# Kernel optimization log

Measured on AMD Instinct MI355X. Metric: run time of the kernel, lower is better.

Reference implementation:

```python
import jax, jax.numpy as jnp
import numpy as np
from jax import lax

EPS = 1e-5
B, CIN, H, W = 2, 2048, 32, 32

def conv2d(x, w, pad):
    return lax.conv_general_dilated(x, w, (1, 1), [(pad, pad), (pad, pad)],
                                    dimension_numbers=('NCHW', 'OIHW', 'NCHW'))

def batchnorm(x, gamma, beta):
    mu = jnp.mean(x, axis=(0, 2, 3), keepdims=True)
    var = jnp.var(x, axis=(0, 2, 3), keepdims=True)
    return (x - mu) * lax.rsqrt(var + EPS) * gamma.reshape(1, -1, 1, 1) + beta.reshape(1, -1, 1, 1)

def deform_conv(x, w_off, w_m, w, k, dil, pad):
    # modulated deformable conv v2: offset conv (3x3) -> 2*k*k, modulation conv -> k*k
    b, c, h, wd = x.shape
    n = k * k
    off = conv2d(x, w_off, 1)                        # [B,2N,H,W]
    mod = jax.nn.sigmoid(conv2d(x, w_m, 1))          # [B,N,H,W]
    off_y = jnp.transpose(off[:, :n], (0, 2, 3, 1))  # [B,H,W,N]
    off_x = jnp.transpose(off[:, n:], (0, 2, 3, 1))
    mod = jnp.transpose(mod, (0, 2, 3, 1))           # [B,H,W,N]
    x_pad = jnp.pad(x, ((0, 0), (0, 0), (pad, pad), (pad, pad)))
    hp, wp = h + 2 * pad, wd + 2 * pad
    taps = (jnp.arange(k) * dil).astype(x.dtype)
    gy = jnp.arange(h, dtype=x.dtype)[:, None] + taps[None, :]   # [H,k] base y in padded coords
    gx = jnp.arange(wd, dtype=x.dtype)[:, None] + taps[None, :]  # [W,k]
    py = (gy[None, :, None, :, None] + off_y.reshape(b, h, wd, k, k)).reshape(b, h, wd, n)
    px = (gx[None, None, :, None, :] + off_x.reshape(b, h, wd, k, k)).reshape(b, h, wd, n)
    py = jnp.clip(py, 0.0, hp - 1)
    px = jnp.clip(px, 0.0, wp - 1)
    y0 = jnp.floor(py); x0 = jnp.floor(px)
    wy = py - y0; wx = px - x0
    y0i = jnp.clip(y0.astype(jnp.int32), 0, hp - 1)
    x0i = jnp.clip(x0.astype(jnp.int32), 0, wp - 1)
    y1i = jnp.clip(y0i + 1, 0, hp - 1)
    x1i = jnp.clip(x0i + 1, 0, wp - 1)
    xf = x_pad.reshape(b, c, hp * wp)
    def gather(yi, xi):
        idx = (yi * wp + xi).reshape(b, -1)               # [B, H*W*N]
        return jax.vmap(lambda f, i: f[:, i])(xf, idx)    # [B, C, H*W*N]
    wy = wy.reshape(b, 1, -1); wx = wx.reshape(b, 1, -1)
    val = ((1 - wy) * (1 - wx) * gather(y0i, x0i)
         + (1 - wy) * wx       * gather(y0i, x1i)
         + wy       * (1 - wx) * gather(y1i, x0i)
         + wy       * wx       * gather(y1i, x1i))
    val = (val * mod.reshape(b, 1, -1)).reshape(b, c, h, wd, n)
    return jnp.einsum('bchwn,ocn->bohw', val, w.reshape(w.shape[0], c, n))

def dspp_forward(x, woff1, wm1, w1, g1, b1, woff2, wm2, w2, g2, b2,
                 woff3, wm3, w3, g3, b3, woff4, wm4, w4, g4, b4,
                 wpool, gp, bp, wfuse, gf, bf):
    x1 = jax.nn.relu(batchnorm(deform_conv(x, woff1, wm1, w1, 1, 1, 0), g1, b1))
    x2 = jax.nn.relu(batchnorm(deform_conv(x, woff2, wm2, w2, 3, 6, 6), g2, b2))
    x3 = jax.nn.relu(batchnorm(deform_conv(x, woff3, wm3, w3, 3, 12, 12), g3, b3))
    x4 = jax.nn.relu(batchnorm(deform_conv(x, woff4, wm4, w4, 3, 18, 18), g4, b4))
    gap = jnp.mean(x, axis=(2, 3))                    # [B,Cin] global avg pool
    p = jnp.einsum('bc,oc->bo', gap, wpool)           # 1x1 conv
    mu = jnp.mean(p, axis=0); var = jnp.var(p, axis=0)
    p = jax.nn.relu((p - mu) * lax.rsqrt(var + EPS) * gp + bp)
    x5 = jnp.broadcast_to(p[:, :, None, None], x4.shape)  # bilinear upsample from 1x1 == broadcast
    cat = jnp.concatenate([x1, x2, x3, x4, x5], axis=1)   # [B,1280,H,W]
    out = jnp.einsum('bchw,oc->bohw', cat, wfuse)
    out = jax.nn.relu(batchnorm(out, gf, bf))
    return out  # dropout is identity at inference


def setup_inputs() -> dict:
    key = jax.random.key(0)
    ks = jax.random.split(key, 16)
    dt = jnp.float32
    def kaiming(k, shape):
        fan_in = int(np.prod(shape[1:]))
        return jax.random.normal(k, shape, dt) * np.float32(np.sqrt(2.0 / fan_in))
    inp = {'x': jax.random.normal(ks[0], (B, CIN, H, W), dt)}
    specs = [(1, 'woff1', 'wm1', 'w1', 'g1', 'b1'),
             (3, 'woff2', 'wm2', 'w2', 'g2', 'b2'),
             (3, 'woff3', 'wm3', 'w3', 'g3', 'b3'),
             (3, 'woff4', 'wm4', 'w4', 'g4', 'b4')]
    i = 1
    for k, no, nm, nw, ng, nb in specs:
        n = k * k
        inp[no] = jax.random.normal(ks[i], (2 * n, CIN, 3, 3), dt) * 0.01; i += 1
        inp[nm] = jax.random.normal(ks[i], (n, CIN, 3, 3), dt) * 0.01; i += 1
        inp[nw] = kaiming(ks[i], (256, CIN, k, k)); i += 1
        inp[ng] = jnp.ones((256,), dt)
        inp[nb] = jnp.zeros((256,), dt)
    inp['wpool'] = kaiming(ks[i], (256, CIN)); i += 1
    inp['gp'] = jnp.ones((256,), dt); inp['bp'] = jnp.zeros((256,), dt)
    inp['wfuse'] = kaiming(ks[i], (256, 1280))
    inp['gf'] = jnp.ones((256,), dt); inp['bf'] = jnp.zeros((256,), dt)
    return inp


def reference(x, woff1, wm1, w1, g1, b1, woff2, wm2, w2, g2, b2,
              woff3, wm3, w3, g3, b3, woff4, wm4, w4, g4, b4,
              wpool, gp, bp, wfuse, gf, bf):
    return dspp_forward(x, woff1, wm1, w1, g1, b1, woff2, wm2, w2, g2, b2,
                        woff3, wm3, w3, g3, b3, woff4, wm4, w4, g4, b4,
                        wpool, gp, bp, wfuse, gf, bf)
```

## Files before the change

### kernel.cpp

```cpp
#include <hip/hip_runtime.h>
#include <hip/hip_fp16.h>
#include <cstdint>
#include <cstddef>

#define EPSV 1e-5f

typedef _Float16 f16x8 __attribute__((ext_vector_type(8)));
typedef float f32x4 __attribute__((ext_vector_type(4)));

__device__ __forceinline__ short f2h(float f) {
    _Float16 h = (_Float16)f;
    union { _Float16 h; short s; } u; u.h = h; return u.s;
}
__device__ __forceinline__ __half2 u2h2(unsigned u) {
    union { unsigned u; __half2 h; } x; x.u = u; return x.h;
}
__device__ __forceinline__ unsigned packh2(float w) {
    _Float16 h = (_Float16)w;
    union { _Float16 h; unsigned short s; } u; u.h = h;
    return (unsigned)u.s * 0x10001u;
}

__global__ void k_zero(float4* p, int n4) {
    int i = blockIdx.x * blockDim.x + threadIdx.x;
    int stride = gridDim.x * blockDim.x;
    for (; i < n4; i += stride) p[i] = float4{0.f, 0.f, 0.f, 0.f};
}

__global__ void k_xpose(const float* __restrict__ x, short* __restrict__ xT) {
    int hw0 = blockIdx.x * 64, c0 = blockIdx.y * 64, b = blockIdx.z;
    __shared__ short tile[64][72];
    int t = threadIdx.x;
    const float* xb = x + (size_t)b * 2048 * 1024;
    int hwi = t & 63, cr = t >> 6;
    #pragma unroll
    for (int r = 0; r < 16; r++) {
        int cl = cr + r * 4;
        tile[hwi][cl] = f2h(xb[(size_t)(c0 + cl) * 1024 + hw0 + hwi]);
    }
    __syncthreads();
    short* xTb = xT + (size_t)b * 1024 * 2048;
    int ci = t & 63, hr = t >> 6;
    #pragma unroll
    for (int r = 0; r < 16; r++) {
        int hwr = hr + r * 4;
        xTb[(size_t)(hw0 + hwr) * 2048 + c0 + ci] = tile[hwr][ci];
    }
}

__global__ void k_convw1(const float* __restrict__ w1, short* __restrict__ A1) {
    int i = blockIdx.x * 256 + threadIdx.x;
    if (i < 256 * 2048) A1[i] = f2h(w1[i]);
}

__global__ void k_convw9(const float* w2, const float* w3, const float* w4,
                         short* A2, short* A3, short* A4) {
    int o = blockIdx.x, cch = blockIdx.y, br = blockIdx.z;
    const float* src = br == 0 ? w2 : br == 1 ? w3 : w4;
    short* dst = br == 0 ? A2 : br == 1 ? A3 : A4;
    __shared__ short lds[4608];
    int t = threadIdx.x;
    const float* basep = src + ((size_t)o * 2048 + cch * 512) * 9;
    #pragma unroll
    for (int s = 0; s < 18; s++) {
        int idx = s * 256 + t;
        int c = idx / 9, jj = idx - c * 9;
        lds[jj * 512 + c] = f2h(basep[idx]);
    }
    __syncthreads();
    short* dbase = dst + (size_t)o * 18432 + cch * 512;
    #pragma unroll
    for (int s = 0; s < 18; s++) {
        int idx = s * 256 + t;
        int jj = idx >> 9, c = idx & 511;
        dbase[(size_t)jj * 2048 + c] = lds[idx];
    }
}

__global__ void k_convoff(const float* woff1, const float* wm1, const float* woff2, const float* wm2,
                          const float* woff3, const float* wm3, const float* woff4, const float* wm4,
                          short* Aoff) {
    int ch = blockIdx.x, cch = blockIdx.y;
    int t = threadIdx.x;
    short* dbase = Aoff + (size_t)ch * 18432 + cch * 512;
    if (ch >= 84) {
        #pragma unroll
        for (int s = 0; s < 18; s++) {
            int idx = s * 256 + t;
            int jj = idx >> 9, c = idx & 511;
            dbase[(size_t)jj * 2048 + c] = 0;
        }
        return;
    }
    const float* src; int oc;
    if (ch < 2)       { src = woff1; oc = ch; }
    else if (ch == 2) { src = wm1;   oc = 0; }
    else if (ch < 21) { src = woff2; oc = ch - 3; }
    else if (ch < 30) { src = wm2;   oc = ch - 21; }
    else if (ch < 48) { src = woff3; oc = ch - 30; }
    else if (ch < 57) { src = wm3;   oc = ch - 48; }
    else if (ch < 75) { src = woff4; oc = ch - 57; }
    else              { src = wm4;   oc = ch - 75; }
    __shared__ short lds[4608];
    const float* basep = src + ((size_t)oc * 2048 + cch * 512) * 9;
    #pragma unroll
    for (int s = 0; s < 18; s++) {
        int idx = s * 256 + t;
        int c = idx / 9, jj = idx - c * 9;
        lds[jj * 512 + c] = f2h(basep[idx]);
    }
    __syncthreads();
    #pragma unroll
    for (int s = 0; s < 18; s++) {
        int idx = s * 256 + t;
        int jj = idx >> 9, c = idx & 511;
        dbase[(size_t)jj * 2048 + c] = lds[idx];
    }
}

__global__ void k_afuse(const float* wfuse, short* Af) {
    int i = blockIdx.x * 256 + threadIdx.x;
    if (i < 256 * 1280) Af[i] = f2h(wfuse[i]);
}

__global__ void k_shtab(int* dtab0) {
    int i = blockIdx.x * 256 + threadIdx.x;
    if (i >= 9 * 2048) return;
    int j = i >> 11, p = i & 2047;
    int hw = p & 1023, h = hw >> 5, w = hw & 31;
    int y = h + j / 3 - 1, xx = w + j % 3 - 1;
    bool v = (y >= 0 && y < 32 && xx >= 0 && xx < 32);
    int4 ii = {v ? y * 32 + xx : 0, 0, 0, 0};
    uint4 ww = {v ? packh2(1.f) : 0u, 0u, 0u, 0u};
    ((int4*)dtab0)[(size_t)i * 2] = ii;
    ((uint4*)dtab0)[(size_t)i * 2 + 1] = ww;
}

__global__ void k_sample(const float* OM, int* dtabi) {
    int i = blockIdx.x * 256 + threadIdx.x;
    if (i >= 57344) return;
    int br, j, p;
    if (i < 2048) { br = 0; j = 0; p = i; }
    else { int r = i - 2048; br = 1 + r / 18432; r %= 18432; j = r >> 11; p = r & 2047; }
    const int dil_[4] = {1, 6, 12, 18};
    const int pad_[4] = {0, 6, 12, 18};
    const int cho_[4] = {0, 3, 30, 57};
    const int chm_[4] = {2, 21, 48, 75};
    const int tbo_[4] = {0, 2048, 20480, 38912};
    int J = br ? 9 : 1;
    int dil = dil_[br], pad = pad_[br];
    int hw = p & 1023, h = hw >> 5, w = hw & 31;
    float offy = OM[(size_t)(cho_[br] + j) * 2048 + p];
    float offx = OM[(size_t)(cho_[br] + J + j) * 2048 + p];
    float mz   = OM[(size_t)(chm_[br] + j) * 2048 + p];
    float m = 1.f / (1.f + expf(-mz));
    int ky = j / 3, kx = j - ky * 3;
    float fh = (float)(h + ky * dil) + offy;
    float fw = (float)(w + kx * dil) + offx;
    int limi = 31 + 2 * pad;
    float lim = (float)limi;
    fh = fminf(fmaxf(fh, 0.f), lim);
    fw = fminf(fmaxf(fw, 0.f), lim);
    float y0f = floorf(fh), x0f = floorf(fw);
    float wy = fh - y0f, wx = fw - x0f;
    int y0 = (int)y0f, x0 = (int)x0f;
    int y1 = min(y0 + 1, limi), x1 = min(x0 + 1, limi);
    int4 ii; uint4 ww;
    {
        int yo = y0 - pad, xo = x0 - pad;
        bool v = ((unsigned)yo < 32u) && ((unsigned)xo < 32u);
        ii.x = v ? yo * 32 + xo : 0; ww.x = v ? packh2((1.f - wy) * (1.f - wx) * m) : 0u;
    }
    {
        int yo = y0 - pad, xo = x1 - pad;
        bool v = ((unsigned)yo < 32u) && ((unsigned)xo < 32u);
        ii.y = v ? yo * 32 + xo : 0; ww.y = v ? packh2((1.f - wy) * wx * m) : 0u;
    }
    {
        int yo = y1 - pad, xo = x0 - pad;
        bool v = ((unsigned)yo < 32u) && ((unsigned)xo < 32u);
        ii.z = v ? yo * 32 + xo : 0; ww.z = v ? packh2(wy * (1.f - wx) * m) : 0u;
    }
    {
        int yo = y1 - pad, xo = x1 - pad;
        bool v = ((unsigned)yo < 32u) && ((unsigned)xo < 32u);
        ii.w = v ? yo * 32 + xo : 0; ww.w = v ? packh2(wy * wx * m) : 0u;
    }
    int ent = tbo_[br] + j * 2048 + p;
    ((int4*)dtabi)[(size_t)ent * 2] = ii;
    ((uint4*)dtabi)[(size_t)ent * 2 + 1] = ww;
}

template <int WM>
__device__ __forceinline__ void gemm_gather_f16(
    const short* __restrict__ A, const int* __restrict__ tab,
    const short* __restrict__ xT, float* __restrict__ C,
    int K, int kbeg, int kend, int nbase)
{
    constexpr int TPB = WM * 128;
    constexpr int TPP = TPB / 128;
    constexpr int CPT = 32 / TPP;
    constexpr int NG = CPT / 8;
    __shared__ __align__(16) short At[WM * 64][40];
    __shared__ __align__(16) short Bt[128][40];
    int t = threadIdx.x;
    f32x4 acc[4][4] = {};

    int p = t / TPP;
    int q = (t % TPP) * CPT;
    int pg = nbase + p;
    int bb = nbase >> 10;
    int jj = kbeg >> 11;
    const int4* te = (const int4*)tab + ((size_t)jj * 2048 + pg) * 2;
    int4 ii = te[0];
    uint4 wp = *(const uint4*)(te + 1);
    __half2 wt0 = u2h2(wp.x), wt1 = u2h2(wp.y), wt2 = u2h2(wp.z), wt3 = u2h2(wp.w);
    const short* xbase = xT + (size_t)bb * 1024 * 2048 + q;
    const short* rp0 = xbase + (size_t)ii.x * 2048;
    const short* rp1 = xbase + (size_t)ii.y * 2048;
    const short* rp2 = xbase + (size_t)ii.z * 2048;
    const short* rp3 = xbase + (size_t)ii.w * 2048;

    int arow = t >> 1;
    int aseg = (t & 1) * 16;
    const short* Ar = A + (size_t)arow * K + aseg;

    int lane = t & 63, wv = t >> 6;
    int mq = (wv >> 1) * 64, nq = (wv & 1) * 64;
    int lm = lane & 15, quad = lane >> 4;

    for (int k0 = kbeg; k0 < kend; k0 += 32) {
        *(uint4*)&At[arow][aseg]     = *(const uint4*)(Ar + k0);
        *(uint4*)&At[arow][aseg + 8] = *(const uint4*)(Ar + k0 + 8);
        {
            int ck = k0 & 2047;
            #pragma unroll
            for (int g = 0; g < NG; g++) {
                __half2 a0 = u2h2(0u), a1 = u2h2(0u), a2 = u2h2(0u), a3 = u2h2(0u);
                int cko = ck + g * 8;
                uint4 d0 = *(const uint4*)(rp0 + cko);
                a0 = __hfma2(u2h2(d0.x), wt0, a0); a1 = __hfma2(u2h2(d0.y), wt0, a1);
                a2 = __hfma2(u2h2(d0.z), wt0, a2); a3 = __hfma2(u2h2(d0.w), wt0, a3);
                uint4 d1 = *(const uint4*)(rp1 + cko);
                a0 = __hfma2(u2h2(d1.x), wt1, a0); a1 = __hfma2(u2h2(d1.y), wt1, a1);
                a2 = __hfma2(u2h2(d1.z), wt1, a2); a3 = __hfma2(u2h2(d1.w), wt1, a3);
                uint4 d2 = *(const uint4*)(rp2 + cko);
                a0 = __hfma2(u2h2(d2.x), wt2, a0); a1 = __hfma2(u2h2(d2.y), wt2, a1);
                a2 = __hfma2(u2h2(d2.z), wt2, a2); a3 = __hfma2(u2h2(d2.w), wt2, a3);
                uint4 d3 = *(const uint4*)(rp3 + cko);
                a0 = __hfma2(u2h2(d3.x), wt3, a0); a1 = __hfma2(u2h2(d3.y), wt3, a1);
                a2 = __hfma2(u2h2(d3.z), wt3, a2); a3 = __hfma2(u2h2(d3.w), wt3, a3);
                union { __half2 h[4]; uint4 u; } pk;
                pk.h[0] = a0; pk.h[1] = a1; pk.h[2] = a2; pk.h[3] = a3;
                *(uint4*)&Bt[p][q + g * 8] = pk.u;
            }
        }
        __syncthreads();
        f16x8 af[4], bfv[4];
        #pragma unroll
        for (int f = 0; f < 4; f++) {
            af[f]  = *(const f16x8*)&At[mq + f * 16 + lm][quad * 8];
            bfv[f] = *(const f16x8*)&Bt[nq + f * 16 + lm][quad * 8];
        }
        #pragma unroll
        for (int fm = 0; fm < 4; fm++)
            #pragma unroll
            for (int fn = 0; fn < 4; fn++)
                acc[fm][fn] = __builtin_amdgcn_mfma_f32_16x16x32_f16(af[fm], bfv[fn], acc[fm][fn], 0, 0, 0);
        __syncthreads();
    }
    #pragma unroll
    for (int fm = 0; fm < 4; fm++) {
        int row0 = mq + fm * 16 + quad * 4;
        #pragma unroll
        for (int fn = 0; fn < 4; fn++) {
            int col = nbase + nq + fn * 16 + lm;
            #pragma unroll
            for (int r = 0; r < 4; r++)
                atomicAdd(&C[(size_t)(row0 + r) * 2048 + col], acc[fm][fn][r]);
        }
    }
}

__global__ __launch_bounds__(256) void k_ogemm(const short* __restrict__ Aoff,
                                               const int* __restrict__ dtab0,
                                               const short* __restrict__ xT,
                                               float* __restrict__ offmod) {
    int kbeg = blockIdx.z * 1024;
    gemm_gather_f16<2>(Aoff, dtab0, xT, offmod, 18432, kbeg, kbeg + 1024, blockIdx.x * 128);
}

__global__ __launch_bounds__(512) void k_dgemm(const short* __restrict__ Aall,
                                               const int* __restrict__ dtab,
                                               const short* __restrict__ xT,
                                               float* __restrict__ ypre) {
    int z = blockIdx.z;
    int br, kbeg;
    if (z < 2) { br = 0; kbeg = z * 1024; }
    else { int zz = z - 2; br = 1 + zz / 18; kbeg = (zz % 18) * 1024; }
    const size_t aoffs[4] = {0, 524288, 524288 + 4718592, 524288 + 2 * (size_t)4718592};
    const int tbo[4] = {0, 2048, 20480, 38912};
    int K = br ? 18432 : 2048;
    gemm_gather_f16<4>(Aall + aoffs[br], dtab + (size_t)tbo[br] * 8, xT,
                       ypre + (size_t)br * 524288, K, kbeg, kbeg + 1024, blockIdx.x * 128);
}

__global__ __launch_bounds__(256) void k_fgemm(const short* __restrict__ A,
                                               const short* __restrict__ Bp,
                                               float* __restrict__ C) {
    __shared__ __align__(16) short At[128][40];
    __shared__ __align__(16) short Bt[128][40];
    int t = threadIdx.x;
    int nbase = blockIdx.x * 128, mbase = blockIdx.y * 128;
    int kbeg = blockIdx.z * 160, kend = kbeg + 160;
    const int K = 1280;
    f32x4 acc[4][4] = {};
    int lane = t & 63, wv = t >> 6;
    int mq = (wv >> 1) * 64, nq = (wv & 1) * 64;
    int lm = lane & 15, quad = lane >> 4;
    for (int k0 = kbeg; k0 < kend; k0 += 32) {
        int row = t >> 2, seg = t & 3;
        *(uint4*)&At[row][seg * 8] = *(const uint4*)(A + (size_t)(mbase + row) * K + k0 + seg * 8);
        *(uint4*)&At[row + 64][seg * 8] = *(const uint4*)(A + (size_t)(mbase + row + 64) * K + k0 + seg * 8);
        *(uint4*)&Bt[row][seg * 8] = *(const uint4*)(Bp + (size_t)(nbase + row) * K + k0 + seg * 8);
        *(uint4*)&Bt[row + 64][seg * 8] = *(const uint4*)(Bp + (size_t)(nbase + row + 64) * K + k0 + seg * 8);
        __syncthreads();
        f16x8 af[4], bfv[4];
        #pragma unroll
        for (int f = 0; f < 4; f++) {
            af[f]  = *(const f16x8*)&At[mq + f * 16 + lm][quad * 8];
            bfv[f] = *(const f16x8*)&Bt[nq + f * 16 + lm][quad * 8];
        }
        #pragma unroll
        for (int fm = 0; fm < 4; fm++)
            #pragma unroll
            for (int fn = 0; fn < 4; fn++)
                acc[fm][fn] = __builtin_amdgcn_mfma_f32_16x16x32_f16(af[fm], bfv[fn], acc[fm][fn], 0, 0, 0);
        __syncthreads();
    }
    #pragma unroll
    for (int fm = 0; fm < 4; fm++) {
        int row0 = mbase + mq + fm * 16 + quad * 4;
        #pragma unroll
        for (int fn = 0; fn < 4; fn++) {
            int col = nbase + nq + fn * 16 + lm;
            #pragma unroll
            for (int r = 0; r < 4; r++)
                atomicAdd(&C[(size_t)(row0 + r) * 2048 + col], acc[fm][fn][r]);
        }
    }
}

__global__ void k_bnstats(const float* Y0, const float* Y1, const float* Y2, const float* Y3,
                          const float* g0, const float* g1, const float* g2, const float* g3,
                          const float* b0, const float* b1, const float* b2, const float* b3,
                          float* S) {
    int br = blockIdx.y;
    const float* Y = br == 0 ? Y0 : br == 1 ? Y1 : br == 2 ? Y2 : Y3;
    const float* g = br == 0 ? g0 : br == 1 ? g1 : br == 2 ? g2 : g3;
    const float* b = br == 0 ? b0 : br == 1 ? b1 : br == 2 ? b2 : b3;
    float* so = S + (size_t)br * 512;
    int o = blockIdx.x, t = threadIdx.x;
    const float* row = Y + (size_t)o * 2048;
    float s = 0.f, ss = 0.f;
    for (int i = t; i < 2048; i += 256) { float v = row[i]; s += v; ss += v * v; }
    #pragma unroll
    for (int off = 32; off; off >>= 1) { s += __shfl_down(s, off); ss += __shfl_down(ss, off); }
    __shared__ float ls[4], lss[4];
    int wv = t >> 6;
    if ((t & 63) == 0) { ls[wv] = s; lss[wv] = ss; }
    __syncthreads();
    if (t == 0) {
        s = ls[0] + ls[1] + ls[2] + ls[3];
        ss = lss[0] + lss[1] + lss[2] + lss[3];
        float mu = s * (1.f / 2048.f);
        float var = ss * (1.f / 2048.f) - mu * mu;
        float sc = g[o] * rsqrtf(var + EPSV);
        so[o] = sc;
        so[256 + o] = b[o] - mu * sc;
    }
}

__global__ void k_gap(const float* X, float* gap) {
    int bc = blockIdx.x;
    const float* row = X + (size_t)bc * 1024;
    int t = threadIdx.x;
    float s = row[t] + row[t + 256] + row[t + 512] + row[t + 768];
    #pragma unroll
    for (int off = 32; off; off >>= 1) s += __shfl_down(s, off);
    __shared__ float ls[4];
    if ((t & 63) == 0) ls[t >> 6] = s;
    __syncthreads();
    if (t == 0) gap[bc] = (ls[0] + ls[1] + ls[2] + ls[3]) * (1.f / 1024.f);
}

__global__ void k_pool(const float* gap, const float* wpool, const float* gp, const float* bp,
                       float* pfin) {
    int o = blockIdx.x, t = threadIdx.x;
    float s0 = 0.f, s1 = 0.f;
    const float* wr = wpool + (size_t)o * 2048;
    for (int c = t; c < 2048; c += 256) {
        float wv = wr[c];
        s0 += wv * gap[c];
        s1 += wv * gap[2048 + c];
    }
    #pragma unroll
    for (int off = 32; off; off >>= 1) { s0 += __shfl_down(s0, off); s1 += __shfl_down(s1, off); }
    __shared__ float l0[4], l1[4];
    int wv_ = t >> 6;
    if ((t & 63) == 0) { l0[wv_] = s0; l1[wv_] = s1; }
    __syncthreads();
    if (t == 0) {
        float p0 = l0[0] + l0[1] + l0[2] + l0[3];
        float p1 = l1[0] + l1[1] + l1[2] + l1[3];
        float mu = 0.5f * (p0 + p1);
        float d0 = p0 - mu, d1 = p1 - mu;
        float var = 0.5f * (d0 * d0 + d1 * d1);
        float r = rsqrtf(var + EPSV);
        pfin[o]       = fmaxf(d0 * r * gp[o] + bp[o], 0.f);
        pfin[256 + o] = fmaxf(d1 * r * gp[o] + bp[o], 0.f);
    }
}

__global__ void k_xcat(const float* __restrict__ ypre, const float* __restrict__ S,
                       const float* __restrict__ pfin, short* __restrict__ xcat) {
    int p0 = blockIdx.x * 64, ct = blockIdx.y;
    int t = threadIdx.x;
    if (ct >= 16) {
        int c0 = 1024 + (ct - 16) * 64;
        int ci = t & 63, pr = t >> 6;
        #pragma unroll
        for (int r = 0; r < 16; r++) {
            int pw = p0 + pr + r * 4;
            int b = pw >> 10;
            xcat[(size_t)pw * 1280 + c0 + ci] = f2h(pfin[b * 256 + (c0 - 1024) + ci]);
        }
        return;
    }
    __shared__ short tile[64][72];
    int c0 = ct * 64;
    int pi = t & 63, cr = t >> 6;
    #pragma unroll
    for (int r = 0; r < 16; r++) {
        int cl = cr + r * 4;
        int cg = c0 + cl;
        int br = cg >> 8, cc = cg & 255;
        float sc = S[br * 512 + cc], sh = S[br * 512 + 256 + cc];
        float v = fmaxf(ypre[(size_t)cg * 2048 + p0 + pi] * sc + sh, 0.f);
        tile[pi][cl] = f2h(v);
    }
    __syncthreads();
    int ci = t & 63, pr = t >> 6;
    #pragma unroll
    for (int r = 0; r < 16; r++) {
        int pw = pr + r * 4;
        xcat[(size_t)(p0 + pw) * 1280 + c0 + ci] = tile[pw][ci];
    }
}

__global__ void k_final(const float* outpre, const float* S, float* dout) {
    int i = blockIdx.x * 256 + threadIdx.x;
    int hw = i & 1023, o = (i >> 10) & 255, b = i >> 18;
    float v = outpre[(size_t)o * 2048 + b * 1024 + hw] * S[o] + S[256 + o];
    dout[i] = fmaxf(v, 0.f);
}

extern "C" void kernel_launch(void* const* d_in, const int* in_sizes, int n_in,
                              void* d_out, int out_size, void* d_ws, size_t ws_size,
                              hipStream_t stream) {
    const float* x     = (const float*)d_in[0];
    const float* woff1 = (const float*)d_in[1];
    const float* wm1   = (const float*)d_in[2];
    const float* w1    = (const float*)d_in[3];
    const float* g1    = (const float*)d_in[4];
    const float* b1    = (const float*)d_in[5];
    const float* woff2 = (const float*)d_in[6];
    const float* wm2   = (const float*)d_in[7];
    const float* w2    = (const float*)d_in[8];
    const float* g2    = (const float*)d_in[9];
    const float* b2    = (const float*)d_in[10];
    const float* woff3 = (const float*)d_in[11];
    const float* wm3   = (const float*)d_in[12];
    const float* w3    = (const float*)d_in[13];
    const float* g3    = (const float*)d_in[14];
    const float* b3    = (const float*)d_in[15];
    const float* woff4 = (const float*)d_in[16];
    const float* wm4   = (const float*)d_in[17];
    const float* w4    = (const float*)d_in[18];
    const float* g4    = (const float*)d_in[19];
    const float* b4    = (const float*)d_in[20];
    const float* wpool = (const float*)d_in[21];
    const float* gp    = (const float*)d_in[22];
    const float* bp    = (const float*)d_in[23];
    const float* wfuse = (const float*)d_in[24];
    const float* gf    = (const float*)d_in[25];
    const float* bf    = (const float*)d_in[26];

    char* ws = (char*)d_ws;
    size_t off = 0;
    auto alloc = [&](size_t bytes) {
        off = (off + 255) & ~(size_t)255;
        size_t o = off; off += bytes; return o;
    };
    size_t off_offmod = alloc(128 * 2048 * 4);
    size_t off_ypre   = alloc((size_t)4 * 256 * 2048 * 4);
    size_t off_outpre = alloc(256 * 2048 * 4);
    size_t off_A1     = alloc((size_t)256 * 2048 * 2);
    size_t off_A2     = alloc((size_t)256 * 18432 * 2);
    size_t off_A3     = alloc((size_t)256 * 18432 * 2);
    size_t off_A4     = alloc((size_t)256 * 18432 * 2);
    size_t off_Aoff   = alloc((size_t)128 * 18432 * 2);
    size_t off_Afuse  = alloc((size_t)256 * 1280 * 2);
    size_t off_xcat   = alloc((size_t)2048 * 1280 * 2);
    size_t off_xT     = alloc((size_t)2 * 1024 * 2048 * 2);
    size_t off_dtab0  = alloc((size_t)9 * 2048 * 32);
    size_t off_dtab   = alloc((size_t)57344 * 32);
    size_t off_scsh   = alloc((size_t)4 * 512 * 4);
    size_t off_scshf  = alloc((size_t)512 * 4);
    size_t off_gap    = alloc((size_t)4096 * 4);
    size_t off_pfin   = alloc((size_t)512 * 4);
    (void)ws_size; (void)in_sizes; (void)n_in; (void)out_size;

    float* offmod = (float*)(ws + off_offmod);
    float* ypre   = (float*)(ws + off_ypre);
    float* outpre = (float*)(ws + off_outpre);
    short* Aall   = (short*)(ws + off_A1);
    short* A1     = (short*)(ws + off_A1);
    short* A2     = (short*)(ws + off_A2);
    short* A3     = (short*)(ws + off_A3);
    short* A4     = (short*)(ws + off_A4);
    short* Aoff   = (short*)(ws + off_Aoff);
    short* Afuse  = (short*)(ws + off_Afuse);
    short* xcat   = (short*)(ws + off_xcat);
    short* xT     = (short*)(ws + off_xT);
    int*   dtab0  = (int*)(ws + off_dtab0);
    int*   dtab   = (int*)(ws + off_dtab);
    float* scsh   = (float*)(ws + off_scsh);
    float* scshf  = (float*)(ws + off_scshf);
    float* gapb   = (float*)(ws + off_gap);
    float* pfin   = (float*)(ws + off_pfin);

    k_zero<<<2048, 256, 0, stream>>>((float4*)(ws + off_offmod), 720896);
    k_xpose<<<dim3(16, 32, 2), 256, 0, stream>>>(x, xT);
    k_convw1<<<2048, 256, 0, stream>>>(w1, A1);
    k_convw9<<<dim3(256, 4, 3), 256, 0, stream>>>(w2, w3, w4, A2, A3, A4);
    k_convoff<<<dim3(128, 4), 256, 0, stream>>>(woff1, wm1, woff2, wm2, woff3, wm3, woff4, wm4, Aoff);
    k_afuse<<<1280, 256, 0, stream>>>(wfuse, Afuse);
    k_shtab<<<72, 256, 0, stream>>>(dtab0);
    k_ogemm<<<dim3(16, 1, 18), 256, 0, stream>>>(Aoff, dtab0, xT, offmod);
    k_sample<<<224, 256, 0, stream>>>(offmod, dtab);
    k_dgemm<<<dim3(16, 1, 56), 512, 0, stream>>>(Aall, dtab, xT, ypre);
    k_bnstats<<<dim3(256, 4), 256, 0, stream>>>(ypre, ypre + 524288, ypre + 2 * 524288, ypre + 3 * 524288,
                                                g1, g2, g3, g4, b1, b2, b3, b4, scsh);
    k_gap<<<4096, 256, 0, stream>>>(x, gapb);
    k_pool<<<256, 256, 0, stream>>>(gapb, wpool, gp, bp, pfin);
    k_xcat<<<dim3(32, 20), 256, 0, stream>>>(ypre, scsh, pfin, xcat);
    k_fgemm<<<dim3(16, 2, 8), 256, 0, stream>>>(Afuse, xcat, outpre);
    k_bnstats<<<dim3(256, 1), 256, 0, stream>>>(outpre, outpre, outpre, outpre,
                                                gf, gf, gf, gf, bf, bf, bf, bf, scshf);
    k_final<<<2048, 256, 0, stream>>>(outpre, scshf, (float*)d_out);
}
```

Baseline: 428.0 us.

## Fuse prep kernels, register-prefetch gather GEMM, specialize offset GEMM taps

Merges the zeroing, weight conversion, transpose, shift-table and global-average-pool kernels into one launch, and folds the pooling branch into the batchnorm stats kernel, cutting the number of launches. The gather GEMM now double-buffers A and gathered-x loads in registers so the next stage's global loads overlap the MFMAs. It also adds a single-tap specialization for the offset GEMM, whose table only has one valid tap, so it skips three gathers. The offset GEMM's K split is doubled and occupancy hints are added, at the cost of higher register pressure and more atomic partial sums.

```diff
diff --git a/kernel.cpp b/kernel.cpp
--- a/kernel.cpp
+++ b/kernel.cpp
@@ -7,6 +7,7 @@
 
 typedef _Float16 f16x8 __attribute__((ext_vector_type(8)));
 typedef float f32x4 __attribute__((ext_vector_type(4)));
+typedef short short4v __attribute__((ext_vector_type(4)));
 
 __device__ __forceinline__ short f2h(float f) {
     _Float16 h = (_Float16)f;
@@ -21,119 +22,143 @@
     return (unsigned)u.s * 0x10001u;
 }
 
-__global__ void k_zero(float4* p, int n4) {
-    int i = blockIdx.x * blockDim.x + threadIdx.x;
-    int stride = gridDim.x * blockDim.x;
-    for (; i < n4; i += stride) p[i] = float4{0.f, 0.f, 0.f, 0.f};
-}
-
-__global__ void k_xpose(const float* __restrict__ x, short* __restrict__ xT) {
-    int hw0 = blockIdx.x * 64, c0 = blockIdx.y * 64, b = blockIdx.z;
-    __shared__ short tile[64][72];
-    int t = threadIdx.x;
-    const float* xb = x + (size_t)b * 2048 * 1024;
-    int hwi = t & 63, cr = t >> 6;
-    #pragma unroll
-    for (int r = 0; r < 16; r++) {
-        int cl = cr + r * 4;
-        tile[hwi][cl] = f2h(xb[(size_t)(c0 + cl) * 1024 + hw0 + hwi]);
-    }
-    __syncthreads();
-    short* xTb = xT + (size_t)b * 1024 * 2048;
-    int ci = t & 63, hr = t >> 6;
-    #pragma unroll
-    for (int r = 0; r < 16; r++) {
-        int hwr = hr + r * 4;
-        xTb[(size_t)(hw0 + hwr) * 2048 + c0 + ci] = tile[hwr][ci];
-    }
-}
-
-__global__ void k_convw1(const float* __restrict__ w1, short* __restrict__ A1) {
-    int i = blockIdx.x * 256 + threadIdx.x;
-    if (i < 256 * 2048) A1[i] = f2h(w1[i]);
-}
-
-__global__ void k_convw9(const float* w2, const float* w3, const float* w4,
-                         short* A2, short* A3, short* A4) {
-    int o = blockIdx.x, cch = blockIdx.y, br = blockIdx.z;
-    const float* src = br == 0 ? w2 : br == 1 ? w3 : w4;
-    short* dst = br == 0 ? A2 : br == 1 ? A3 : A4;
-    __shared__ short lds[4608];
-    int t = threadIdx.x;
-    const float* basep = src + ((size_t)o * 2048 + cch * 512) * 9;
-    #pragma unroll
-    for (int s = 0; s < 18; s++) {
-        int idx = s * 256 + t;
-        int c = idx / 9, jj = idx - c * 9;
-        lds[jj * 512 + c] = f2h(basep[idx]);
-    }
-    __syncthreads();
-    short* dbase = dst + (size_t)o * 18432 + cch * 512;
-    #pragma unroll
-    for (int s = 0; s < 18; s++) {
-        int idx = s * 256 + t;
-        int jj = idx >> 9, c = idx & 511;
-        dbase[(size_t)jj * 2048 + c] = lds[idx];
-    }
-}
-
-__global__ void k_convoff(const float* woff1, const float* wm1, const float* woff2, const float* wm2,
-                          const float* woff3, const float* wm3, const float* woff4, const float* wm4,
-                          short* Aoff) {
-    int ch = blockIdx.x, cch = blockIdx.y;
-    int t = threadIdx.x;
-    short* dbase = Aoff + (size_t)ch * 18432 + cch * 512;
-    if (ch >= 84) {
+__global__ __launch_bounds__(256) void k_prep(
+    const float* __restrict__ x, short* __restrict__ xT,
+    const float* __restrict__ w1, short* __restrict__ A1,
+    const float* __restrict__ wfuse, short* __restrict__ Af,
+    int* __restrict__ dtab0,
+    const float* __restrict__ woff1, const float* __restrict__ wm1,
+    const float* __restrict__ woff2, const float* __restrict__ wm2,
+    const float* __restrict__ woff3, const float* __restrict__ wm3,
+    const float* __restrict__ woff4, const float* __restrict__ wm4,
+    short* __restrict__ Aoff,
+    const float* __restrict__ w2, const float* __restrict__ w3, const float* __restrict__ w4,
+    short* __restrict__ A2, short* __restrict__ A3, short* __restrict__ A4,
+    float4* __restrict__ zbase, float* __restrict__ gap)
+{
+    __shared__ short lds9[4608];
+    __shared__ float lsg[4];
+    int bx = blockIdx.x, t = threadIdx.x;
+    if (bx < 1024) {
+        for (int i = bx * 256 + t; i < 720896; i += 262144)
+            zbase[i] = float4{0.f, 0.f, 0.f, 0.f};
+        return;
+    }
+    if (bx < 1536) {
+        int i4 = (bx - 1024) * 256 + t;
+        float4 v = ((const float4*)w1)[i4];
+        ((short4v*)A1)[i4] = short4v{f2h(v.x), f2h(v.y), f2h(v.z), f2h(v.w)};
+        return;
+    }
+    if (bx < 1856) {
+        int i4 = (bx - 1536) * 256 + t;
+        float4 v = ((const float4*)wfuse)[i4];
+        ((short4v*)Af)[i4] = short4v{f2h(v.x), f2h(v.y), f2h(v.z), f2h(v.w)};
+        return;
+    }
+    if (bx < 1928) {
+        int i = (bx - 1856) * 256 + t;
+        if (i >= 9 * 2048) return;
+        int j = i >> 11, p = i & 2047;
+        int hw = p & 1023, h = hw >> 5, w = hw & 31;
+        int y = h + j / 3 - 1, xx = w + j % 3 - 1;
+        bool v = (y >= 0 && y < 32 && xx >= 0 && xx < 32);
+        int4 ii = {v ? y * 32 + xx : 0, 0, 0, 0};
+        uint4 ww = {v ? packh2(1.f) : 0u, 0u, 0u, 0u};
+        ((int4*)dtab0)[(size_t)i * 2] = ii;
+        ((uint4*)dtab0)[(size_t)i * 2 + 1] = ww;
+        return;
+    }
+    if (bx < 2440) {
+        int qb = bx - 1928;
+        int ch = qb >> 2, cch = qb & 3;
+        short* dbase = Aoff + (size_t)ch * 18432 + cch * 512;
+        if (ch >= 84) {
+            #pragma unroll
+            for (int s = 0; s < 18; s++) {
+                int idx = s * 256 + t;
+                int jj = idx >> 9, c = idx & 511;
+                dbase[(size_t)jj * 2048 + c] = 0;
+            }
+            return;
+        }
+        const float* src; int oc;
+        if (ch < 2)       { src = woff1; oc = ch; }
+        else if (ch == 2) { src = wm1;   oc = 0; }
+        else if (ch < 21) { src = woff2; oc = ch - 3; }
+        else if (ch < 30) { src = wm2;   oc = ch - 21; }
+        else if (ch < 48) { src = woff3; oc = ch - 30; }
+        else if (ch < 57) { src = wm3;   oc = ch - 48; }
+        else if (ch < 75) { src = woff4; oc = ch - 57; }
+        else              { src = wm4;   oc = ch - 75; }
+        const float* basep = src + ((size_t)oc * 2048 + cch * 512) * 9;
+        #pragma unroll
+        for (int s = 0; s < 18; s++) {
+            int idx = s * 256 + t;
+            int c = idx / 9, jj = idx - c * 9;
+            lds9[jj * 512 + c] = f2h(basep[idx]);
+        }
+        __syncthreads();
         #pragma unroll
         for (int s = 0; s < 18; s++) {
             int idx = s * 256 + t;
             int jj = idx >> 9, c = idx & 511;
-            dbase[(size_t)jj * 2048 + c] = 0;
-        }
-        return;
-    }
-    const float* src; int oc;
-    if (ch < 2)       { src = woff1; oc = ch; }
-    else if (ch == 2) { src = wm1;   oc = 0; }
-    else if (ch < 21) { src = woff2; oc = ch - 3; }
-    else if (ch < 30) { src = wm2;   oc = ch - 21; }
-    else if (ch < 48) { src = woff3; oc = ch - 30; }
-    else if (ch < 57) { src = wm3;   oc = ch - 48; }
-    else if (ch < 75) { src = woff4; oc = ch - 57; }
-    else              { src = wm4;   oc = ch - 75; }
-    __shared__ short lds[4608];
-    const float* basep = src + ((size_t)oc * 2048 + cch * 512) * 9;
-    #pragma unroll
-    for (int s = 0; s < 18; s++) {
-        int idx = s * 256 + t;
-        int c = idx / 9, jj = idx - c * 9;
-        lds[jj * 512 + c] = f2h(basep[idx]);
-    }
-    __syncthreads();
-    #pragma unroll
-    for (int s = 0; s < 18; s++) {
-        int idx = s * 256 + t;
-        int jj = idx >> 9, c = idx & 511;
-        dbase[(size_t)jj * 2048 + c] = lds[idx];
-    }
-}
-
-__global__ void k_afuse(const float* wfuse, short* Af) {
-    int i = blockIdx.x * 256 + threadIdx.x;
-    if (i < 256 * 1280) Af[i] = f2h(wfuse[i]);
-}
-
-__global__ void k_shtab(int* dtab0) {
-    int i = blockIdx.x * 256 + threadIdx.x;
-    if (i >= 9 * 2048) return;
-    int j = i >> 11, p = i & 2047;
-    int hw = p & 1023, h = hw >> 5, w = hw & 31;
-    int y = h + j / 3 - 1, xx = w + j % 3 - 1;
-    bool v = (y >= 0 && y < 32 && xx >= 0 && xx < 32);
-    int4 ii = {v ? y * 32 + xx : 0, 0, 0, 0};
-    uint4 ww = {v ? packh2(1.f) : 0u, 0u, 0u, 0u};
-    ((int4*)dtab0)[(size_t)i * 2] = ii;
-    ((uint4*)dtab0)[(size_t)i * 2 + 1] = ww;
+            dbase[(size_t)jj * 2048 + c] = lds9[idx];
+        }
+        return;
+    }
+    if (bx < 5512) {
+        int qb = bx - 2440;
+        int o = qb & 255, cch = (qb >> 8) & 3, br = qb >> 10;
+        const float* src = br == 0 ? w2 : br == 1 ? w3 : w4;
+        short* dst = br == 0 ? A2 : br == 1 ? A3 : A4;
+        const float* basep = src + ((size_t)o * 2048 + cch * 512) * 9;
+        #pragma unroll
+        for (int s = 0; s < 18; s++) {
+            int idx = s * 256 + t;
+            int c = idx / 9, jj = idx - c * 9;
+            lds9[jj * 512 + c] = f2h(basep[idx]);
+        }
+        __syncthreads();
+        short* dbase = dst + (size_t)o * 18432 + cch * 512;
+        #pragma unroll
+        for (int s = 0; s < 18; s++) {
+            int idx = s * 256 + t;
+            int jj = idx >> 9, c = idx & 511;
+            dbase[(size_t)jj * 2048 + c] = lds9[idx];
+        }
+        return;
+    }
+    if (bx < 6536) {
+        int qb = bx - 5512;
+        int hw0 = (qb & 15) * 64, c0 = ((qb >> 4) & 31) * 64, b = qb >> 9;
+        const float* xb = x + (size_t)b * 2048 * 1024;
+        int hwi = t & 63, cr = t >> 6;
+        #pragma unroll
+        for (int r = 0; r < 16; r++) {
+            int cl = cr + r * 4;
+            lds9[hwi * 72 + cl] = f2h(xb[(size_t)(c0 + cl) * 1024 + hw0 + hwi]);
+        }
+        __syncthreads();
+        short* xTb = xT + (size_t)b * 1024 * 2048;
+        int ci = t & 63, hr = t >> 6;
+        #pragma unroll
+        for (int r = 0; r < 16; r++) {
+            int hwr = hr + r * 4;
+            xTb[(size_t)(hw0 + hwr) * 2048 + c0 + ci] = lds9[hwr * 72 + ci];
+        }
+        return;
+    }
+    {
+        int bc = bx - 6536;
+        const float* row = x + (size_t)bc * 1024;
+        float s = row[t] + row[t + 256] + row[t + 512] + row[t + 768];
+        #pragma unroll
+        for (int off = 32; off; off >>= 1) s += __shfl_down(s, off);
+        if ((t & 63) == 0) lsg[t >> 6] = s;
+        __syncthreads();
+        if (t == 0) gap[bc] = (lsg[0] + lsg[1] + lsg[2] + lsg[3]) * (1.f / 1024.f);
+    }
 }
 
 __global__ void k_sample(const float* OM, int* dtabi) {
@@ -191,14 +216,13 @@
     ((uint4*)dtabi)[(size_t)ent * 2 + 1] = ww;
 }
 
-template <int WM>
+template <int WM, int NTAP>
 __device__ __forceinline__ void gemm_gather_f16(
     const short* __restrict__ A, const int* __restrict__ tab,
     const short* __restrict__ xT, float* __restrict__ C,
     int K, int kbeg, int kend, int nbase)
 {
-    constexpr int TPB = WM * 128;
-    constexpr int TPP = TPB / 128;
+    constexpr int TPP = WM;
     constexpr int CPT = 32 / TPP;
     constexpr int NG = CPT / 8;
     __shared__ __align__(16) short At[WM * 64][40];
@@ -229,46 +253,81 @@
     int mq = (wv >> 1) * 64, nq = (wv & 1) * 64;
     int lm = lane & 15, quad = lane >> 4;
 
-    for (int k0 = kbeg; k0 < kend; k0 += 32) {
-        *(uint4*)&At[arow][aseg]     = *(const uint4*)(Ar + k0);
-        *(uint4*)&At[arow][aseg + 8] = *(const uint4*)(Ar + k0 + 8);
-        {
-            int ck = k0 & 2047;
-            #pragma unroll
-            for (int g = 0; g < NG; g++) {
-                __half2 a0 = u2h2(0u), a1 = u2h2(0u), a2 = u2h2(0u), a3 = u2h2(0u);
-                int cko = ck + g * 8;
-                uint4 d0 = *(const uint4*)(rp0 + cko);
-                a0 = __hfma2(u2h2(d0.x), wt0, a0); a1 = __hfma2(u2h2(d0.y), wt0, a1);
-                a2 = __hfma2(u2h2(d0.z), wt0, a2); a3 = __hfma2(u2h2(d0.w), wt0, a3);
-                uint4 d1 = *(const uint4*)(rp1 + cko);
-                a0 = __hfma2(u2h2(d1.x), wt1, a0); a1 = __hfma2(u2h2(d1.y), wt1, a1);
-                a2 = __hfma2(u2h2(d1.z), wt1, a2); a3 = __hfma2(u2h2(d1.w), wt1, a3);
-                uint4 d2 = *(const uint4*)(rp2 + cko);
-                a0 = __hfma2(u2h2(d2.x), wt2, a0); a1 = __hfma2(u2h2(d2.y), wt2, a1);
-                a2 = __hfma2(u2h2(d2.z), wt2, a2); a3 = __hfma2(u2h2(d2.w), wt2, a3);
-                uint4 d3 = *(const uint4*)(rp3 + cko);
-                a0 = __hfma2(u2h2(d3.x), wt3, a0); a1 = __hfma2(u2h2(d3.y), wt3, a1);
-                a2 = __hfma2(u2h2(d3.z), wt3, a2); a3 = __hfma2(u2h2(d3.w), wt3, a3);
-                union { __half2 h[4]; uint4 u; } pk;
-                pk.h[0] = a0; pk.h[1] = a1; pk.h[2] = a2; pk.h[3] = a3;
-                *(uint4*)&Bt[p][q + g * 8] = pk.u;
-            }
-        }
-        __syncthreads();
-        f16x8 af[4], bfv[4];
-        #pragma unroll
-        for (int f = 0; f < 4; f++) {
-            af[f]  = *(const f16x8*)&At[mq + f * 16 + lm][quad * 8];
-            bfv[f] = *(const f16x8*)&Bt[nq + f * 16 + lm][quad * 8];
-        }
-        #pragma unroll
-        for (int fm = 0; fm < 4; fm++)
-            #pragma unroll
-            for (int fn = 0; fn < 4; fn++)
-                acc[fm][fn] = __builtin_amdgcn_mfma_f32_16x16x32_f16(af[fm], bfv[fn], acc[fm][fn], 0, 0, 0);
-        __syncthreads();
-    }
+    uint4 Aa[2], Ab[2];
+    uint4 G0[2][NG], G1[2][NG], G2[2][NG], G3[2][NG];
+
+#define LDSTAGE(S, KK) { \
+    int ck_ = (KK) & 2047; \
+    Aa[S] = *(const uint4*)(Ar + (KK)); \
+    Ab[S] = *(const uint4*)(Ar + (KK) + 8); \
+    _Pragma("unroll") \
+    for (int g = 0; g < NG; g++) { \
+        int o8_ = ck_ + g * 8; \
+        G0[S][g] = *(const uint4*)(rp0 + o8_); \
+        if (NTAP == 4) { \
+            G1[S][g] = *(const uint4*)(rp1 + o8_); \
+            G2[S][g] = *(const uint4*)(rp2 + o8_); \
+            G3[S][g] = *(const uint4*)(rp3 + o8_); \
+        } \
+    } }
+
+#define STEP(S, KPRE) { \
+    uint4 pk[NG]; \
+    _Pragma("unroll") \
+    for (int g = 0; g < NG; g++) { \
+        __half2 r0 = __hmul2(u2h2(G0[S][g].x), wt0); \
+        __half2 r1 = __hmul2(u2h2(G0[S][g].y), wt0); \
+        __half2 r2 = __hmul2(u2h2(G0[S][g].z), wt0); \
+        __half2 r3 = __hmul2(u2h2(G0[S][g].w), wt0); \
+        if (NTAP == 4) { \
+            r0 = __hfma2(u2h2(G1[S][g].x), wt1, r0); \
+            r1 = __hfma2(u2h2(G1[S][g].y), wt1, r1); \
+            r2 = __hfma2(u2h2(G1[S][g].z), wt1, r2); \
+            r3 = __hfma2(u2h2(G1[S][g].w), wt1, r3); \
+            r0 = __hfma2(u2h2(G2[S][g].x), wt2, r0); \
+            r1 = __hfma2(u2h2(G2[S][g].y), wt2, r1); \
+            r2 = __hfma2(u2h2(G2[S][g].z), wt2, r2); \
+            r3 = __hfma2(u2h2(G2[S][g].w), wt2, r3); \
+            r0 = __hfma2(u2h2(G3[S][g].x), wt3, r0); \
+            r1 = __hfma2(u2h2(G3[S][g].y), wt3, r1); \
+            r2 = __hfma2(u2h2(G3[S][g].z), wt3, r2); \
+            r3 = __hfma2(u2h2(G3[S][g].w), wt3, r3); \
+        } \
+        union { __half2 h[4]; uint4 u; } uu; \
+        uu.h[0] = r0; uu.h[1] = r1; uu.h[2] = r2; uu.h[3] = r3; \
+        pk[g] = uu.u; \
+    } \
+    __syncthreads(); \
+    *(uint4*)&At[arow][aseg]     = Aa[S]; \
+    *(uint4*)&At[arow][aseg + 8] = Ab[S]; \
+    _Pragma("unroll") \
+    for (int g = 0; g < NG; g++) *(uint4*)&Bt[p][q + g * 8] = pk[g]; \
+    LDSTAGE(S, KPRE); \
+    __syncthreads(); \
+    f16x8 af[4], bfv[4]; \
+    _Pragma("unroll") \
+    for (int f = 0; f < 4; f++) { \
+        af[f]  = *(const f16x8*)&At[mq + f * 16 + lm][quad * 8]; \
+        bfv[f] = *(const f16x8*)&Bt[nq + f * 16 + lm][quad * 8]; \
+    } \
+    _Pragma("unroll") \
+    for (int fm = 0; fm < 4; fm++) \
+        _Pragma("unroll") \
+        for (int fn = 0; fn < 4; fn++) \
+            acc[fm][fn] = __builtin_amdgcn_mfma_f32_16x16x32_f16(af[fm], bfv[fn], acc[fm][fn], 0, 0, 0); \
+}
+
+    LDSTAGE(0, kbeg);
+    LDSTAGE(1, kbeg + 32);
+    for (int k0 = kbeg; k0 < kend; k0 += 64) {
+        int kp0 = k0 + 64; if (kp0 >= kend) kp0 = kbeg;
+        int kp1 = k0 + 96; if (kp1 >= kend) kp1 = kbeg;
+        STEP(0, kp0);
+        STEP(1, kp1);
+    }
+#undef LDSTAGE
+#undef STEP
+
     #pragma unroll
     for (int fm = 0; fm < 4; fm++) {
         int row0 = mq + fm * 16 + quad * 4;
@@ -282,18 +341,18 @@
     }
 }
 
-__global__ __launch_bounds__(256) void k_ogemm(const short* __restrict__ Aoff,
-                                               const int* __restrict__ dtab0,
-                                               const short* __restrict__ xT,
-                                               float* __restrict__ offmod) {
-    int kbeg = blockIdx.z * 1024;
-    gemm_gather_f16<2>(Aoff, dtab0, xT, offmod, 18432, kbeg, kbeg + 1024, blockIdx.x * 128);
-}
-
-__global__ __launch_bounds__(512) void k_dgemm(const short* __restrict__ Aall,
-                                               const int* __restrict__ dtab,
-                                               const short* __restrict__ xT,
-                                               float* __restrict__ ypre) {
+__global__ __launch_bounds__(256, 4) void k_ogemm(const short* __restrict__ Aoff,
+                                                  const int* __restrict__ dtab0,
+                                                  const short* __restrict__ xT,
+                                                  float* __restrict__ offmod) {
+    int kbeg = blockIdx.z * 512;
+    gemm_gather_f16<2, 1>(Aoff, dtab0, xT, offmod, 18432, kbeg, kbeg + 512, blockIdx.x * 128);
+}
+
+__global__ __launch_bounds__(512, 4) void k_dgemm(const short* __restrict__ Aall,
+                                                  const int* __restrict__ dtab,
+                                                  const short* __restrict__ xT,
+                                                  float* __restrict__ ypre) {
     int z = blockIdx.z;
     int br, kbeg;
     if (z < 2) { br = 0; kbeg = z * 1024; }
@@ -301,8 +360,8 @@
     const size_t aoffs[4] = {0, 524288, 524288 + 4718592, 524288 + 2 * (size_t)4718592};
     const int tbo[4] = {0, 2048, 20480, 38912};
     int K = br ? 18432 : 2048;
-    gemm_gather_f16<4>(Aall + aoffs[br], dtab + (size_t)tbo[br] * 8, xT,
-                       ypre + (size_t)br * 524288, K, kbeg, kbeg + 1024, blockIdx.x * 128);
+    gemm_gather_f16<4, 4>(Aall + aoffs[br], dtab + (size_t)tbo[br] * 8, xT,
+                          ypre + (size_t)br * 524288, K, kbeg, kbeg + 1024, blockIdx.x * 128);
 }
 
 __global__ __launch_bounds__(256) void k_fgemm(const short* __restrict__ A,
@@ -351,74 +410,60 @@
     }
 }
 
-__global__ void k_bnstats(const float* Y0, const float* Y1, const float* Y2, const float* Y3,
-                          const float* g0, const float* g1, const float* g2, const float* g3,
-                          const float* b0, const float* b1, const float* b2, const float* b3,
-                          float* S) {
+__global__ void k_bnpool(const float* Y0, const float* Y1, const float* Y2, const float* Y3,
+                         const float* g0, const float* g1, const float* g2, const float* g3,
+                         const float* b0, const float* b1, const float* b2, const float* b3,
+                         float* S,
+                         const float* gap, const float* wpool, const float* gp,
+                         const float* bp, float* pfin) {
     int br = blockIdx.y;
+    int o = blockIdx.x, t = threadIdx.x;
+    __shared__ float l0[4], l1[4];
+    if (br == 4) {
+        float s0 = 0.f, s1 = 0.f;
+        const float* wr = wpool + (size_t)o * 2048;
+        for (int c = t; c < 2048; c += 256) {
+            float wv = wr[c];
+            s0 += wv * gap[c];
+            s1 += wv * gap[2048 + c];
+        }
+        #pragma unroll
+        for (int off = 32; off; off >>= 1) { s0 += __shfl_down(s0, off); s1 += __shfl_down(s1, off); }
+        int wv_ = t >> 6;
+        if ((t & 63) == 0) { l0[wv_] = s0; l1[wv_] = s1; }
+        __syncthreads();
+        if (t == 0) {
+            float p0 = l0[0] + l0[1] + l0[2] + l0[3];
+            float p1 = l1[0] + l1[1] + l1[2] + l1[3];
+            float mu = 0.5f * (p0 + p1);
+            float d0 = p0 - mu, d1 = p1 - mu;
+            float var = 0.5f * (d0 * d0 + d1 * d1);
+            float r = rsqrtf(var + EPSV);
+            pfin[o]       = fmaxf(d0 * r * gp[o] + bp[o], 0.f);
+            pfin[256 + o] = fmaxf(d1 * r * gp[o] + bp[o], 0.f);
+        }
+        return;
+    }
     const float* Y = br == 0 ? Y0 : br == 1 ? Y1 : br == 2 ? Y2 : Y3;
     const float* g = br == 0 ? g0 : br == 1 ? g1 : br == 2 ? g2 : g3;
     const float* b = br == 0 ? b0 : br == 1 ? b1 : br == 2 ? b2 : b3;
     float* so = S + (size_t)br * 512;
-    int o = blockIdx.x, t = threadIdx.x;
     const float* row = Y + (size_t)o * 2048;
     float s = 0.f, ss = 0.f;
     for (int i = t; i < 2048; i += 256) { float v = row[i]; s += v; ss += v * v; }
     #pragma unroll
     for (int off = 32; off; off >>= 1) { s += __shfl_down(s, off); ss += __shfl_down(ss, off); }
-    __shared__ float ls[4], lss[4];
     int wv = t >> 6;
-    if ((t & 63) == 0) { ls[wv] = s; lss[wv] = ss; }
+    if ((t & 63) == 0) { l0[wv] = s; l1[wv] = ss; }
     __syncthreads();
     if (t == 0) {
-        s = ls[0] + ls[1] + ls[2] + ls[3];
-        ss = lss[0] + lss[1] + lss[2] + lss[3];
+        s = l0[0] + l0[1] + l0[2] + l0[3];
+        ss = l1[0] + l1[1] + l1[2] + l1[3];
         float mu = s * (1.f / 2048.f);
         float var = ss * (1.f / 2048.f) - mu * mu;
         float sc = g[o] * rsqrtf(var + EPSV);
         so[o] = sc;
         so[256 + o] = b[o] - mu * sc;
-    }
-}
-
-__global__ void k_gap(const float* X, float* gap) {
-    int bc = blockIdx.x;
-    const float* row = X + (size_t)bc * 1024;
-    int t = threadIdx.x;
-    float s = row[t] + row[t + 256] + row[t + 512] + row[t + 768];
-    #pragma unroll
-    for (int off = 32; off; off >>= 1) s += __shfl_down(s, off);
-    __shared__ float ls[4];
-    if ((t & 63) == 0) ls[t >> 6] = s;
-    __syncthreads();
-    if (t == 0) gap[bc] = (ls[0] + ls[1] + ls[2] + ls[3]) * (1.f / 1024.f);
-}
-
-__global__ void k_pool(const float* gap, const float* wpool, const float* gp, const float* bp,
-                       float* pfin) {
-    int o = blockIdx.x, t = threadIdx.x;
-    float s0 = 0.f, s1 = 0.f;
-    const float* wr = wpool + (size_t)o * 2048;
-    for (int c = t; c < 2048; c += 256) {
-        float wv = wr[c];
-        s0 += wv * gap[c];
-        s1 += wv * gap[2048 + c];
-    }
-    #pragma unroll
-    for (int off = 32; off; off >>= 1) { s0 += __shfl_down(s0, off); s1 += __shfl_down(s1, off); }
-    __shared__ float l0[4], l1[4];
-    int wv_ = t >> 6;
-    if ((t & 63) == 0) { l0[wv_] = s0; l1[wv_] = s1; }
-    __syncthreads();
-    if (t == 0) {
-        float p0 = l0[0] + l0[1] + l0[2] + l0[3];
-        float p1 = l1[0] + l1[1] + l1[2] + l1[3];
-        float mu = 0.5f * (p0 + p1);
-        float d0 = p0 - mu, d1 = p1 - mu;
-        float var = 0.5f * (d0 * d0 + d1 * d1);
-        float r = rsqrtf(var + EPSV);
-        pfin[o]       = fmaxf(d0 * r * gp[o] + bp[o], 0.f);
-        pfin[256 + o] = fmaxf(d1 * r * gp[o] + bp[o], 0.f);
     }
 }
 
@@ -540,23 +585,20 @@
     float* gapb   = (float*)(ws + off_gap);
     float* pfin   = (float*)(ws + off_pfin);
 
-    k_zero<<<2048, 256, 0, stream>>>((float4*)(ws + off_offmod), 720896);
-    k_xpose<<<dim3(16, 32, 2), 256, 0, stream>>>(x, xT);
-    k_convw1<<<2048, 256, 0, stream>>>(w1, A1);
-    k_convw9<<<dim3(256, 4, 3), 256, 0, stream>>>(w2, w3, w4, A2, A3, A4);
-    k_convoff<<<dim3(128, 4), 256, 0, stream>>>(woff1, wm1, woff2, wm2, woff3, wm3, woff4, wm4, Aoff);
-    k_afuse<<<1280, 256, 0, stream>>>(wfuse, Afuse);
-    k_shtab<<<72, 256, 0, stream>>>(dtab0);
-    k_ogemm<<<dim3(16, 1, 18), 256, 0, stream>>>(Aoff, dtab0, xT, offmod);
+    k_prep<<<10632, 256, 0, stream>>>(x, xT, w1, A1, wfuse, Afuse, dtab0,
+                                      woff1, wm1, woff2, wm2, woff3, wm3, woff4, wm4, Aoff,
+                                      w2, w3, w4, A2, A3, A4,
+                                      (float4*)(ws + off_offmod), gapb);
+    k_ogemm<<<dim3(16, 1, 36), 256, 0, stream>>>(Aoff, dtab0, xT, offmod);
     k_sample<<<224, 256, 0, stream>>>(offmod, dtab);
     k_dgemm<<<dim3(16, 1, 56), 512, 0, stream>>>(Aall, dtab, xT, ypre);
-    k_bnstats<<<dim3(256, 4), 256, 0, stream>>>(ypre, ypre + 524288, ypre + 2 * 524288, ypre + 3 * 524288,
-                                                g1, g2, g3, g4, b1, b2, b3, b4, scsh);
-    k_gap<<<4096, 256, 0, stream>>>(x, gapb);
-    k_pool<<<256, 256, 0, stream>>>(gapb, wpool, gp, bp, pfin);
+    k_bnpool<<<dim3(256, 5), 256, 0, stream>>>(ypre, ypre + 524288, ypre + 2 * 524288, ypre + 3 * 524288,
+                                               g1, g2, g3, g4, b1, b2, b3, b4, scsh,
+                                               gapb, wpool, gp, bp, pfin);
     k_xcat<<<dim3(32, 20), 256, 0, stream>>>(ypre, scsh, pfin, xcat);
     k_fgemm<<<dim3(16, 2, 8), 256, 0, stream>>>(Afuse, xcat, outpre);
-    k_bnstats<<<dim3(256, 1), 256, 0, stream>>>(outpre, outpre, outpre, outpre,
-                                                gf, gf, gf, gf, bf, bf, bf, bf, scshf);
+    k_bnpool<<<dim3(256, 1), 256, 0, stream>>>(outpre, outpre, outpre, outpre,
+                                               gf, gf, gf, gf, bf, bf, bf, bf, scshf,
+                                               gapb, wpool, gp, bp, pfin);
     k_final<<<2048, 256, 0, stream>>>(outpre, scshf, (float*)d_out);
 }
```

Result: slower. 749.7 us (+75.2%).
